# Kernel optimization log

Hardware: AMD Instinct MI355X
Metric: run time of the kernel (lower is better)

Reference implementation:

```python
import jax, jax.numpy as jnp
import numpy as np

LOG_2PI = np.float32(np.log(2.0 * np.pi))
NEG_BIG = np.float32(-9e15)


def setup_inputs() -> dict:
    key = jax.random.key(0)
    ks = jax.random.split(key, 8)
    N, F_in, F_out, H = 8192, 512, 128, 16
    x = jax.random.normal(ks[0], (N, F_in), dtype=jnp.float32)
    adj = jax.random.randint(ks[1], (N, N), 0, 2, dtype=jnp.int32)
    # xavier_uniform-ish init for W (gain 1.414)
    lim = np.float32(1.414 * np.sqrt(6.0 / (F_in + F_out)))
    W = jax.random.uniform(ks[2], (F_in, F_out), jnp.float32, -lim, lim)
    # VariationalAttentionNet params: lin1(2*F_out -> H), lin21/lin22(H -> 1)
    w1 = jax.random.normal(ks[3], (H, 2 * F_out), dtype=jnp.float32) * 0.05
    b1 = jnp.zeros((H,), jnp.float32)
    w21 = jax.random.normal(ks[4], (1, H), dtype=jnp.float32) * 0.05
    b21 = jnp.zeros((1,), jnp.float32)
    w22 = jax.random.normal(ks[5], (1, H), dtype=jnp.float32) * 0.05
    b22 = jnp.zeros((1,), jnp.float32)
    return {"x": x, "adj": adj, "W": W, "w1": w1, "b1": b1,
            "w21": w21, "b21": b21, "w22": w22, "b22": b22}


def reference(x, adj, W, w1, b1, w21, b21, w22, b22):
    # h = x @ W  [N, F_out]
    h = x @ W
    # VariationalAttentionNet(h, h), eval mode: z = mu
    u = jax.nn.relu(jnp.concatenate([h, h], axis=1) @ w1.T + b1)  # [N, H]
    mu = u @ w21.T + b21   # [N, 1]
    lv = u @ w22.T + b22   # [N, 1]
    sigma = jax.nn.softplus(lv)
    z = mu
    # qmp = -(log p(z) - log q(z)); with z = mu, log q(mu) = -log(sigma) - 0.5*log(2pi)
    log_p = jnp.sum(-0.5 * z * z - 0.5 * LOG_2PI)
    log_q = jnp.sum(-jnp.log(sigma) - 0.5 * LOG_2PI)
    qmp = log_q - log_p
    # per-node score z broadcast across row, masked by adjacency, row softmax
    scores = jnp.where(adj > 0, z, NEG_BIG)          # [N, N]
    attention = jax.nn.softmax(scores, axis=1)       # [N, N] (dropout off in eval)
    h_prime = attention @ h                          # [N, F_out]
    return jax.nn.elu(h_prime), qmp
```

## Files before the change

kernel.cpp:

```cpp
#include <hip/hip_runtime.h>

typedef unsigned int u32;
typedef unsigned short u16;

#define NN 8192
#define FIN 512
#define FOUT 128
#define NH 16
#define BK 64

typedef float f32x16 __attribute__((ext_vector_type(16)));
typedef __bf16 bf16x8 __attribute__((ext_vector_type(8)));

union PackAB { u32 u[4]; bf16x8 v; };

__device__ __forceinline__ u32 rne_hi(u32 u) {
  return u + (0x7FFFu + ((u >> 16) & 1u));
}
__device__ __forceinline__ u16 f32_to_bf16(float f) {
  return (u16)(rne_hi(__float_as_uint(f)) >> 16);
}

__global__ __launch_bounds__(256) void prep_kernel(
    const float* __restrict__ W, const float* __restrict__ w1,
    u16* __restrict__ WT, float* __restrict__ w1s) {
  int b = blockIdx.x, t = threadIdx.x;
  if (b < 256) {
    int o = b * 256 + t;
    int n = o >> 9, k = o & 511;
    WT[o] = f32_to_bf16(W[k * FOUT + n]);
  } else {
    for (int e = t; e < NH * FOUT; e += 256) {
      int k = e >> 7, f = e & 127;
      w1s[e] = w1[k * 256 + f] + w1[k * 256 + 128 + f];
    }
  }
}

__global__ __launch_bounds__(256, 6) void h_kernel(
    const float* __restrict__ x, const u16* __restrict__ WT,
    float* __restrict__ Hp, int KL) {
  __shared__ u16 aS[32 * BK];
  __shared__ u16 bS[128 * BK];
  int t = threadIdx.x;
  int w = t >> 6, l = t & 63;
  int m = l & 31, kh = l >> 5;
  int tile = blockIdx.x & 255, chunk = blockIdx.x >> 8;
  int i0 = tile * 32, k0 = chunk * KL;

  int arow = t >> 4, acol = (t & 15) * 4;
  int ac = (t & 15) >> 1, ah = t & 1;
  int aoff0 = arow * BK + ((ac ^ (arow & 7)) << 3) + ah * 4;
  int aoff1 = (arow + 16) * BK + ((ac ^ ((arow + 16) & 7)) << 3) + ah * 4;
  const float* ap0 = x + (size_t)(i0 + arow) * FIN + k0 + acol;
  const float* ap1 = ap0 + (size_t)16 * FIN;
  int hr = t >> 3, hc = t & 7;
  const u16* bp0 = WT + (size_t)hr * FIN + k0 + hc * 8;
  int boff[4];
#pragma unroll
  for (int p = 0; p < 4; ++p) {
    int r = hr + 32 * p;
    boff[p] = r * BK + ((hc ^ (r & 7)) << 3);
  }
  int aro = m * BK, am7 = m & 7;
  int nB = w * 32 + m;
  int bro = nB * BK, bm7 = nB & 7;

  f32x16 acc;
#pragma unroll
  for (int r = 0; r < 16; ++r) acc[r] = 0.0f;

  for (int o = 0; o < KL; o += BK) {
    float4 a0 = *(const float4*)ap0;
    float4 a1 = *(const float4*)ap1;
    uint4 h0 = *(const uint4*)bp0;
    uint4 h1 = *(const uint4*)(bp0 + 32 * (size_t)FIN);
    uint4 h2 = *(const uint4*)(bp0 + 64 * (size_t)FIN);
    uint4 h3 = *(const uint4*)(bp0 + 96 * (size_t)FIN);
    ap0 += BK; ap1 += BK; bp0 += BK;
    uint2 w0, w1v;
    w0.x = (rne_hi(__float_as_uint(a0.y)) & 0xFFFF0000u) | (rne_hi(__float_as_uint(a0.x)) >> 16);
    w0.y = (rne_hi(__float_as_uint(a0.w)) & 0xFFFF0000u) | (rne_hi(__float_as_uint(a0.z)) >> 16);
    w1v.x = (rne_hi(__float_as_uint(a1.y)) & 0xFFFF0000u) | (rne_hi(__float_as_uint(a1.x)) >> 16);
    w1v.y = (rne_hi(__float_as_uint(a1.w)) & 0xFFFF0000u) | (rne_hi(__float_as_uint(a1.z)) >> 16);
    *(uint2*)&aS[aoff0] = w0;
    *(uint2*)&aS[aoff1] = w1v;
    *(uint4*)&bS[boff[0]] = h0;
    *(uint4*)&bS[boff[1]] = h1;
    *(uint4*)&bS[boff[2]] = h2;
    *(uint4*)&bS[boff[3]] = h3;
    __syncthreads();
#pragma unroll
    for (int s = 0; s < BK; s += 16) {
      int cA = (s >> 3) + kh;
      PackAB pa, pb;
      pa.v = *(const bf16x8*)&aS[aro + ((cA ^ am7) << 3)];
      pb.v = *(const bf16x8*)&bS[bro + ((cA ^ bm7) << 3)];
      acc = __builtin_amdgcn_mfma_f32_32x32x16_bf16(pa.v, pb.v, acc, 0, 0, 0);
    }
    __syncthreads();
  }
  float* hp = Hp + (size_t)chunk * NN * FOUT;
  int col = w * 32 + m;
#pragma unroll
  for (int r = 0; r < 16; ++r) {
    int row = (r & 3) + 8 * (r >> 2) + 4 * kh;
    hp[(size_t)(i0 + row) * FOUT + col] = acc[r];
  }
}

__global__ __launch_bounds__(256) void reduceH_kernel(
    const float* __restrict__ Hp, int KSH,
    const float* __restrict__ b1, const float* __restrict__ w21,
    const float* __restrict__ b21, const float* __restrict__ w22,
    const float* __restrict__ b22, const float* __restrict__ w1s,
    u16* __restrict__ HT, float* __restrict__ qpart) {
  __shared__ float hs[32][FOUT + 4];
  __shared__ float w1l[NH][FOUT + 4];
  __shared__ float us[32][NH + 1];
  int t = threadIdx.x;
  int i0 = blockIdx.x * 32;
  float v[16];
  const float* base = Hp + (size_t)i0 * FOUT + t * 16;
#pragma unroll
  for (int e = 0; e < 16; e += 4) {
    float4 x4 = *(const float4*)(base + e);
    v[e] = x4.x; v[e + 1] = x4.y; v[e + 2] = x4.z; v[e + 3] = x4.w;
  }
  for (int c = 1; c < KSH; ++c) {
    const float* p = base + (size_t)c * NN * FOUT;
#pragma unroll
    for (int e = 0; e < 16; e += 4) {
      float4 x4 = *(const float4*)(p + e);
      v[e] += x4.x; v[e + 1] += x4.y; v[e + 2] += x4.z; v[e + 3] += x4.w;
    }
  }
  {
    int row = t >> 3, c0 = (t & 7) * 16;
#pragma unroll
    for (int e = 0; e < 16; ++e) hs[row][c0 + e] = v[e];
  }
  for (int e = t; e < NH * FOUT; e += 256) w1l[e >> 7][e & 127] = w1s[e];
  __syncthreads();
#pragma unroll
  for (int cc = 0; cc < 2; ++cc) {
    int c = cc * 64 + (t >> 2), q = t & 3;
    u32 p[4];
#pragma unroll
    for (int j = 0; j < 4; ++j) {
      u16 lo = f32_to_bf16(hs[q * 8 + 2 * j][c]);
      u16 hi = f32_to_bf16(hs[q * 8 + 2 * j + 1][c]);
      p[j] = (u32)lo | ((u32)hi << 16);
    }
    uint4 st; st.x = p[0]; st.y = p[1]; st.z = p[2]; st.w = p[3];
    *(uint4*)(HT + (size_t)c * NN + i0 + q * 8) = st;
  }
  {
    int i = t >> 3, p = t & 7;
    float s0 = b1[p], s1 = b1[p + 8];
#pragma unroll 4
    for (int f = 0; f < FOUT; ++f) {
      float hv = hs[i][f];
      s0 = fmaf(hv, w1l[p][f], s0);
      s1 = fmaf(hv, w1l[p + 8][f], s1);
    }
    us[i][p] = fmaxf(s0, 0.0f);
    us[i][p + 8] = fmaxf(s1, 0.0f);
  }
  __syncthreads();
  if (t < 32) {
    float mu = b21[0], lv = b22[0];
#pragma unroll
    for (int k = 0; k < NH; ++k) {
      mu = fmaf(us[t][k], w21[k], mu);
      lv = fmaf(us[t][k], w22[k], lv);
    }
    float sp = fmaxf(lv, 0.0f) + log1pf(expf(-fabsf(lv)));
    float q = 0.5f * mu * mu - logf(sp);
#pragma unroll
    for (int off = 16; off; off >>= 1) q += __shfl_down(q, off);
    if (t == 0) qpart[blockIdx.x] = q;
  }
}

__global__ __launch_bounds__(256, 6) void attn_kernel(
    const int* __restrict__ adj, const u16* __restrict__ HT,
    float* __restrict__ Sp, u32* __restrict__ degw, int KL) {
  __shared__ u16 aS[32 * BK];
  __shared__ u16 bS[128 * BK];
  int t = threadIdx.x;
  int w = t >> 6, l = t & 63;
  int m = l & 31, kh = l >> 5;
  int tile = blockIdx.x & 255, chunk = blockIdx.x >> 8;
  int i0 = tile * 32, k0 = chunk * KL;
  int nslab = KL / BK;

  int arow = t >> 4, acol = (t & 15) * 4;
  int ac = (t & 15) >> 1, ah = t & 1;
  int aoff0 = arow * BK + ((ac ^ (arow & 7)) << 3) + ah * 4;
  int aoff1 = (arow + 16) * BK + ((ac ^ ((arow + 16) & 7)) << 3) + ah * 4;
  const int* apb = adj + (size_t)(i0 + arow) * NN + k0 + acol;
  int hr = t >> 3, hc = t & 7;
  const u16* bpb = HT + (size_t)hr * NN + k0 + hc * 8;
  int boff[4];
#pragma unroll
  for (int p = 0; p < 4; ++p) {
    int r = hr + 32 * p;
    boff[p] = r * BK + ((hc ^ (r & 7)) << 3);
  }
  int aro = m * BK, am7 = m & 7;
  int nB = w * 32 + m;
  int bro = nB * BK, bm7 = nB & 7;

  f32x16 acc;
#pragma unroll
  for (int r = 0; r < 16; ++r) acc[r] = 0.0f;
  u32 degA = 0, degB = 0;

  int sl = tile % nslab;
  int4 a0 = *(const int4*)(apb + (size_t)sl * BK);
  int4 a1 = *(const int4*)(apb + (size_t)sl * BK + (size_t)16 * NN);
  uint4 h0 = *(const uint4*)(bpb + (size_t)sl * BK);
  uint4 h1 = *(const uint4*)(bpb + (size_t)sl * BK + 32 * (size_t)NN);
  uint4 h2 = *(const uint4*)(bpb + (size_t)sl * BK + 64 * (size_t)NN);
  uint4 h3 = *(const uint4*)(bpb + (size_t)sl * BK + 96 * (size_t)NN);

  for (int oo = 0; oo < nslab; ++oo) {
    u32 p00 = ((u32)a0.y << 16) | (u32)a0.x;
    u32 p01 = ((u32)a0.w << 16) | (u32)a0.z;
    u32 p10 = ((u32)a1.y << 16) | (u32)a1.x;
    u32 p11 = ((u32)a1.w << 16) | (u32)a1.z;
    degA += p00 + p01;
    degB += p10 + p11;
    uint2 w0, w1v;
    w0.x = p00 * 0x3F80u; w0.y = p01 * 0x3F80u;
    w1v.x = p10 * 0x3F80u; w1v.y = p11 * 0x3F80u;
    *(uint2*)&aS[aoff0] = w0;
    *(uint2*)&aS[aoff1] = w1v;
    *(uint4*)&bS[boff[0]] = h0;
    *(uint4*)&bS[boff[1]] = h1;
    *(uint4*)&bS[boff[2]] = h2;
    *(uint4*)&bS[boff[3]] = h3;
    __syncthreads();
    if (oo + 1 < nslab) {
      int s2 = sl + 1 == nslab ? 0 : sl + 1;
      sl = s2;
      a0 = *(const int4*)(apb + (size_t)s2 * BK);
      a1 = *(const int4*)(apb + (size_t)s2 * BK + (size_t)16 * NN);
      h0 = *(const uint4*)(bpb + (size_t)s2 * BK);
      h1 = *(const uint4*)(bpb + (size_t)s2 * BK + 32 * (size_t)NN);
      h2 = *(const uint4*)(bpb + (size_t)s2 * BK + 64 * (size_t)NN);
      h3 = *(const uint4*)(bpb + (size_t)s2 * BK + 96 * (size_t)NN);
    }
#pragma unroll
    for (int s = 0; s < BK; s += 16) {
      int cA = (s >> 3) + kh;
      PackAB pa, pb;
      pa.v = *(const bf16x8*)&aS[aro + ((cA ^ am7) << 3)];
      pb.v = *(const bf16x8*)&bS[bro + ((cA ^ bm7) << 3)];
      acc = __builtin_amdgcn_mfma_f32_32x32x16_bf16(pa.v, pb.v, acc, 0, 0, 0);
    }
    __syncthreads();
  }
  u32 dA = (degA & 0xFFFFu) + (degA >> 16);
  u32 dB = (degB & 0xFFFFu) + (degB >> 16);
#pragma unroll
  for (int off = 8; off; off >>= 1) {
    dA += __shfl_down(dA, off);
    dB += __shfl_down(dB, off);
  }
  if ((t & 15) == 0) {
    degw[chunk * NN + i0 + arow] = dA;
    degw[chunk * NN + i0 + arow + 16] = dB;
  }
  float* sp = Sp + (size_t)chunk * NN * FOUT;
  int col = w * 32 + m;
#pragma unroll
  for (int r = 0; r < 16; ++r) {
    int row = (r & 3) + 8 * (r >> 2) + 4 * kh;
    sp[(size_t)(i0 + row) * FOUT + col] = acc[r];
  }
}

__global__ __launch_bounds__(256) void reduceSq_kernel(
    const float* __restrict__ Sp, const u32* __restrict__ degw,
    const float* __restrict__ qpart, float* __restrict__ out, int KSA) {
  int t = threadIdx.x;
  if (blockIdx.x == 1024) {
    __shared__ float sred[4];
    float v = qpart[t];
#pragma unroll
    for (int off = 32; off; off >>= 1) v += __shfl_down(v, off);
    if ((t & 63) == 0) sred[t >> 6] = v;
    __syncthreads();
    if (t == 0) out[(size_t)NN * FOUT] = sred[0] + sred[1] + sred[2] + sred[3];
    return;
  }
  int idx = (blockIdx.x * 256 + t) * 4;
  int i = idx >> 7;
  u32 deg = 0;
  for (int c = 0; c < KSA; ++c) deg += degw[c * NN + i];
  float4 s = {0.0f, 0.0f, 0.0f, 0.0f};
  for (int c = 0; c < KSA; ++c) {
    float4 v4 = *(const float4*)(Sp + (size_t)c * NN * FOUT + idx);
    s.x += v4.x; s.y += v4.y; s.z += v4.z; s.w += v4.w;
  }
  float rd = deg ? 1.0f / (float)deg : 0.0f;
  float4 o;
  o.x = s.x * rd; o.y = s.y * rd; o.z = s.z * rd; o.w = s.w * rd;
  o.x = o.x > 0.0f ? o.x : expm1f(o.x);
  o.y = o.y > 0.0f ? o.y : expm1f(o.y);
  o.z = o.z > 0.0f ? o.z : expm1f(o.z);
  o.w = o.w > 0.0f ? o.w : expm1f(o.w);
  *(float4*)(out + idx) = o;
}

extern "C" void kernel_launch(void* const* d_in, const int* in_sizes, int n_in,
                              void* d_out, int out_size, void* d_ws, size_t ws_size,
                              hipStream_t stream) {
  (void)in_sizes; (void)n_in; (void)out_size;
  const float* x   = (const float*)d_in[0];
  const int*   adj = (const int*)d_in[1];
  const float* W   = (const float*)d_in[2];
  const float* w1  = (const float*)d_in[3];
  const float* b1  = (const float*)d_in[4];
  const float* w21 = (const float*)d_in[5];
  const float* b21 = (const float*)d_in[6];
  const float* w22 = (const float*)d_in[7];
  const float* b22 = (const float*)d_in[8];
  float* out = (float*)d_out;

  const size_t TILE4 = (size_t)NN * FOUT * 4;
  int KSA = 8, KSH = 4;
  for (;;) {
    size_t need = (size_t)(KSA + KSH) * TILE4
                + (size_t)NN * FOUT * 2
                + (size_t)FOUT * FIN * 2
                + (size_t)KSA * NN * 4
                + NH * FOUT * 4 + 2048;
    if (need <= ws_size || (KSA == 1 && KSH == 1)) break;
    if (KSH > 1) KSH >>= 1; else KSA >>= 1;
  }

  char* ws = (char*)d_ws;
  float* Sp   = (float*)ws;                          ws += (size_t)KSA * TILE4;
  float* Hp   = (float*)ws;                          ws += (size_t)KSH * TILE4;
  u16*   HT   = (u16*)ws;                            ws += (size_t)NN * FOUT * 2;
  u16*   WT   = (u16*)ws;                            ws += (size_t)FOUT * FIN * 2;
  u32*   degw = (u32*)ws;                            ws += (size_t)KSA * NN * 4;
  float* w1s  = (float*)ws;                          ws += NH * FOUT * 4;
  float* qpart= (float*)ws;

  prep_kernel<<<257, 256, 0, stream>>>(W, w1, WT, w1s);
  h_kernel<<<256 * KSH, 256, 0, stream>>>(x, WT, Hp, FIN / KSH);
  reduceH_kernel<<<256, 256, 0, stream>>>(Hp, KSH, b1, w21, b21, w22, b22, w1s, HT, qpart);
  attn_kernel<<<256 * KSA, 256, 0, stream>>>(adj, HT, Sp, degw, NN / KSA);
  reduceSq_kernel<<<1025, 256, 0, stream>>>(Sp, degw, qpart, out, KSA);
}
```

Measured before the change: 437.3 us.

## Store H in MFMA fragment layout and read B operand directly from global

reduceH now writes the bf16 H matrix pre-swizzled into the exact per-lane MFMA B-fragment order, so attn_kernel loads B operands straight from global/L2 instead of staging them through shared memory. The attention kernel uses a wider 256-column adjacency slab with only A in LDS, drops the register-prefetch double buffering, and halves the K split count. This removes LDS traffic and barriers for H but relies on cache hits for B reads and loses explicit overlap of adjacency loads with MFMA.

```diff
diff --git a/kernel.cpp b/kernel.cpp
--- a/kernel.cpp
+++ b/kernel.cpp
@@ -8,6 +8,7 @@
 #define FOUT 128
 #define NH 16
 #define BK 64
+#define BKA 256
 
 typedef float f32x16 __attribute__((ext_vector_type(16)));
 typedef __bf16 bf16x8 __attribute__((ext_vector_type(8)));
@@ -114,7 +115,7 @@
     const float* __restrict__ b1, const float* __restrict__ w21,
     const float* __restrict__ b21, const float* __restrict__ w22,
     const float* __restrict__ b22, const float* __restrict__ w1s,
-    u16* __restrict__ HT, float* __restrict__ qpart) {
+    u16* __restrict__ HTf, float* __restrict__ qpart) {
   __shared__ float hs[32][FOUT + 4];
   __shared__ float w1l[NH][FOUT + 4];
   __shared__ float us[32][NH + 1];
@@ -142,18 +143,23 @@
   }
   for (int e = t; e < NH * FOUT; e += 256) w1l[e >> 7][e & 127] = w1s[e];
   __syncthreads();
-#pragma unroll
-  for (int cc = 0; cc < 2; ++cc) {
-    int c = cc * 64 + (t >> 2), q = t & 3;
-    u32 p[4];
-#pragma unroll
-    for (int j = 0; j < 4; ++j) {
-      u16 lo = f32_to_bf16(hs[q * 8 + 2 * j][c]);
-      u16 hi = f32_to_bf16(hs[q * 8 + 2 * j + 1][c]);
-      p[j] = (u32)lo | ((u32)hi << 16);
-    }
-    uint4 st; st.x = p[0]; st.y = p[1]; st.z = p[2]; st.w = p[3];
-    *(uint4*)(HT + (size_t)c * NN + i0 + q * 8) = st;
+  {
+    int n = t & 127, g2 = t >> 7;
+#pragma unroll
+    for (int gg = 0; gg < 2; ++gg) {
+      int g = g2 + 2 * gg;
+      int k16 = (i0 >> 4) + (g >> 1), kh = g & 1;
+      u32 p[4];
+#pragma unroll
+      for (int j = 0; j < 4; ++j) {
+        u16 lo = f32_to_bf16(hs[g * 8 + 2 * j][n]);
+        u16 hi = f32_to_bf16(hs[g * 8 + 2 * j + 1][n]);
+        p[j] = (u32)lo | ((u32)hi << 16);
+      }
+      uint4 st; st.x = p[0]; st.y = p[1]; st.z = p[2]; st.w = p[3];
+      size_t off = ((size_t)(k16 * 4 + (n >> 5)) * 64 + kh * 32 + (n & 31)) * 8;
+      *(uint4*)(HTf + off) = st;
+    }
   }
   {
     int i = t >> 3, p = t & 7;
@@ -183,96 +189,62 @@
   }
 }
 
-__global__ __launch_bounds__(256, 6) void attn_kernel(
-    const int* __restrict__ adj, const u16* __restrict__ HT,
+__global__ __launch_bounds__(256, 4) void attn_kernel(
+    const int* __restrict__ adj, const u16* __restrict__ HTf,
     float* __restrict__ Sp, u32* __restrict__ degw, int KL) {
-  __shared__ u16 aS[32 * BK];
-  __shared__ u16 bS[128 * BK];
+  __shared__ u16 aS[32 * BKA];
   int t = threadIdx.x;
   int w = t >> 6, l = t & 63;
   int m = l & 31, kh = l >> 5;
   int tile = blockIdx.x & 255, chunk = blockIdx.x >> 8;
   int i0 = tile * 32, k0 = chunk * KL;
-  int nslab = KL / BK;
-
-  int arow = t >> 4, acol = (t & 15) * 4;
-  int ac = (t & 15) >> 1, ah = t & 1;
-  int aoff0 = arow * BK + ((ac ^ (arow & 7)) << 3) + ah * 4;
-  int aoff1 = (arow + 16) * BK + ((ac ^ ((arow + 16) & 7)) << 3) + ah * 4;
-  const int* apb = adj + (size_t)(i0 + arow) * NN + k0 + acol;
-  int hr = t >> 3, hc = t & 7;
-  const u16* bpb = HT + (size_t)hr * NN + k0 + hc * 8;
-  int boff[4];
-#pragma unroll
-  for (int p = 0; p < 4; ++p) {
-    int r = hr + 32 * p;
-    boff[p] = r * BK + ((hc ^ (r & 7)) << 3);
-  }
-  int aro = m * BK, am7 = m & 7;
-  int nB = w * 32 + m;
-  int bro = nB * BK, bm7 = nB & 7;
+
+  int ar = t >> 3, lc = t & 7;
+  const int* apb = adj + (size_t)(i0 + ar) * NN + k0 + lc * 4;
+  int woff[8];
+#pragma unroll
+  for (int q = 0; q < 8; ++q) {
+    int c = q * 4 + (lc >> 1);
+    woff[q] = ar * 256 + ((c ^ ar) << 3) + (lc & 1) * 4;
+  }
+  const u16* bp = HTf + ((size_t)(k0 >> 4) * 4 * 64 + (size_t)(w * 64 + l)) * 8;
 
   f32x16 acc;
 #pragma unroll
   for (int r = 0; r < 16; ++r) acc[r] = 0.0f;
-  u32 degA = 0, degB = 0;
-
-  int sl = tile % nslab;
-  int4 a0 = *(const int4*)(apb + (size_t)sl * BK);
-  int4 a1 = *(const int4*)(apb + (size_t)sl * BK + (size_t)16 * NN);
-  uint4 h0 = *(const uint4*)(bpb + (size_t)sl * BK);
-  uint4 h1 = *(const uint4*)(bpb + (size_t)sl * BK + 32 * (size_t)NN);
-  uint4 h2 = *(const uint4*)(bpb + (size_t)sl * BK + 64 * (size_t)NN);
-  uint4 h3 = *(const uint4*)(bpb + (size_t)sl * BK + 96 * (size_t)NN);
-
-  for (int oo = 0; oo < nslab; ++oo) {
-    u32 p00 = ((u32)a0.y << 16) | (u32)a0.x;
-    u32 p01 = ((u32)a0.w << 16) | (u32)a0.z;
-    u32 p10 = ((u32)a1.y << 16) | (u32)a1.x;
-    u32 p11 = ((u32)a1.w << 16) | (u32)a1.z;
-    degA += p00 + p01;
-    degB += p10 + p11;
-    uint2 w0, w1v;
-    w0.x = p00 * 0x3F80u; w0.y = p01 * 0x3F80u;
-    w1v.x = p10 * 0x3F80u; w1v.y = p11 * 0x3F80u;
-    *(uint2*)&aS[aoff0] = w0;
-    *(uint2*)&aS[aoff1] = w1v;
-    *(uint4*)&bS[boff[0]] = h0;
-    *(uint4*)&bS[boff[1]] = h1;
-    *(uint4*)&bS[boff[2]] = h2;
-    *(uint4*)&bS[boff[3]] = h3;
+  u32 degacc = 0;
+
+  int nslab = KL / BKA;
+  for (int o = 0; o < nslab; ++o) {
+    int4 aR[8];
+#pragma unroll
+    for (int q = 0; q < 8; ++q) aR[q] = *(const int4*)(apb + q * 32);
+    apb += BKA;
+    if (o) __syncthreads();
+#pragma unroll
+    for (int q = 0; q < 8; ++q) {
+      u32 p0 = ((u32)aR[q].y << 16) | (u32)aR[q].x;
+      u32 p1 = ((u32)aR[q].w << 16) | (u32)aR[q].z;
+      degacc += p0 + p1;
+      uint2 wv; wv.x = p0 * 0x3F80u; wv.y = p1 * 0x3F80u;
+      *(uint2*)&aS[woff[q]] = wv;
+    }
     __syncthreads();
-    if (oo + 1 < nslab) {
-      int s2 = sl + 1 == nslab ? 0 : sl + 1;
-      sl = s2;
-      a0 = *(const int4*)(apb + (size_t)s2 * BK);
-      a1 = *(const int4*)(apb + (size_t)s2 * BK + (size_t)16 * NN);
-      h0 = *(const uint4*)(bpb + (size_t)s2 * BK);
-      h1 = *(const uint4*)(bpb + (size_t)s2 * BK + 32 * (size_t)NN);
-      h2 = *(const uint4*)(bpb + (size_t)s2 * BK + 64 * (size_t)NN);
-      h3 = *(const uint4*)(bpb + (size_t)s2 * BK + 96 * (size_t)NN);
-    }
-#pragma unroll
-    for (int s = 0; s < BK; s += 16) {
-      int cA = (s >> 3) + kh;
-      PackAB pa, pb;
-      pa.v = *(const bf16x8*)&aS[aro + ((cA ^ am7) << 3)];
-      pb.v = *(const bf16x8*)&bS[bro + ((cA ^ bm7) << 3)];
-      acc = __builtin_amdgcn_mfma_f32_32x32x16_bf16(pa.v, pb.v, acc, 0, 0, 0);
-    }
-    __syncthreads();
-  }
-  u32 dA = (degA & 0xFFFFu) + (degA >> 16);
-  u32 dB = (degB & 0xFFFFu) + (degB >> 16);
-#pragma unroll
-  for (int off = 8; off; off >>= 1) {
-    dA += __shfl_down(dA, off);
-    dB += __shfl_down(dB, off);
-  }
-  if ((t & 15) == 0) {
-    degw[chunk * NN + i0 + arow] = dA;
-    degw[chunk * NN + i0 + arow + 16] = dB;
-  }
+#pragma unroll
+    for (int k16 = 0; k16 < 16; ++k16) {
+      PackAB pa, pb2;
+      pb2.v = *(const bf16x8*)(bp + (size_t)k16 * 2048);
+      int c = k16 * 2 + kh;
+      pa.v = *(const bf16x8*)&aS[m * 256 + ((c ^ m) << 3)];
+      acc = __builtin_amdgcn_mfma_f32_32x32x16_bf16(pa.v, pb2.v, acc, 0, 0, 0);
+    }
+    bp += (size_t)16 * 2048;
+  }
+  u32 d = (degacc & 0xFFFFu) + (degacc >> 16);
+  d += __shfl_down(d, 4);
+  d += __shfl_down(d, 2);
+  d += __shfl_down(d, 1);
+  if (lc == 0) degw[chunk * NN + i0 + ar] = d;
   float* sp = Sp + (size_t)chunk * NN * FOUT;
   int col = w * 32 + m;
 #pragma unroll
@@ -331,7 +303,7 @@
   float* out = (float*)d_out;
 
   const size_t TILE4 = (size_t)NN * FOUT * 4;
-  int KSA = 8, KSH = 4;
+  int KSA = 4, KSH = 4;
   for (;;) {
     size_t need = (size_t)(KSA + KSH) * TILE4
                 + (size_t)NN * FOUT * 2
@@ -345,7 +317,7 @@
   char* ws = (char*)d_ws;
   float* Sp   = (float*)ws;                          ws += (size_t)KSA * TILE4;
   float* Hp   = (float*)ws;                          ws += (size_t)KSH * TILE4;
-  u16*   HT   = (u16*)ws;                            ws += (size_t)NN * FOUT * 2;
+  u16*   HTf  = (u16*)ws;                            ws += (size_t)NN * FOUT * 2;
   u16*   WT   = (u16*)ws;                            ws += (size_t)FOUT * FIN * 2;
   u32*   degw = (u32*)ws;                            ws += (size_t)KSA * NN * 4;
   float* w1s  = (float*)ws;                          ws += NH * FOUT * 4;
@@ -353,7 +325,7 @@
 
   prep_kernel<<<257, 256, 0, stream>>>(W, w1, WT, w1s);
   h_kernel<<<256 * KSH, 256, 0, stream>>>(x, WT, Hp, FIN / KSH);
-  reduceH_kernel<<<256, 256, 0, stream>>>(Hp, KSH, b1, w21, b21, w22, b22, w1s, HT, qpart);
-  attn_kernel<<<256 * KSA, 256, 0, stream>>>(adj, HT, Sp, degw, NN / KSA);
+  reduceH_kernel<<<256, 256, 0, stream>>>(Hp, KSH, b1, w21, b21, w22, b22, w1s, HTf, qpart);
+  attn_kernel<<<256 * KSA, 256, 0, stream>>>(adj, HTf, Sp, degw, NN / KSA);
   reduceSq_kernel<<<1025, 256, 0, stream>>>(Sp, degw, qpart, out, KSA);
 }
```

After: 423.2 us. -3.2%, faster.
